# Performance work log

Measured on AMD Instinct MI355X. Metric: run time of the kernel, lower is better.

## Reference

```python
import jax, jax.numpy as jnp
import numpy as np

D_MODEL = 1024
D_HEAD = 64
RANK = 8
LEAF = 4
NUM_LEAVES = D_HEAD // LEAF            # 16
NUM_LEVELS = 4                          # log2(64/4)
BLOCK_SIZES = [4, 8, 16, 32]
RANKS = [min(RANK, b) for b in BLOCK_SIZES]   # [4,8,8,8]
NUM_NODES = [NUM_LEAVES // 2 ** (l + 1) for l in range(NUM_LEVELS)]  # [8,4,2,1]


def _elu1(x):
    return jax.nn.elu(x) + 1.0


def setup_inputs() -> dict:
    key = jax.random.key(0)
    ks = jax.random.split(key, 32)
    B, T = 8, 2048
    x = jax.random.normal(ks[0], (B, T, D_MODEL), jnp.float32)
    s_in = 1.0 / np.sqrt(D_MODEL)
    s_out = 1.0 / np.sqrt(D_HEAD)
    inp = {
        'x': x,
        'Wq': jax.random.normal(ks[1], (D_MODEL, D_HEAD), jnp.float32) * s_in,
        'Wk': jax.random.normal(ks[2], (D_MODEL, D_HEAD), jnp.float32) * s_in,
        'Wv': jax.random.normal(ks[3], (D_MODEL, D_HEAD), jnp.float32) * s_in,
        'Wo': jax.random.normal(ks[4], (D_HEAD, D_MODEL), jnp.float32) * s_out,
    }
    # Fixed orthonormal bases per level (torch.linalg.qr of randn in original)
    idx = 5
    for name in ['UL', 'VR', 'UR', 'VL']:
        for l in range(NUM_LEVELS):
            bs, rl = BLOCK_SIZES[l], RANKS[l]
            Q, _ = jnp.linalg.qr(jax.random.normal(ks[idx], (bs, rl), jnp.float32))
            inp[f'{name}{l}'] = Q
            idx += 1
    return inp


def _hss_forward(x, Wq, Wk, Wv, Wo, UL, VR, UR, VL):
    B, T, _ = x.shape
    q = _elu1(x @ Wq)   # (B,T,Dh)
    k = _elu1(x @ Wk)
    v = x @ Wv

    leaf0 = jnp.zeros((B, NUM_LEAVES, LEAF, LEAF), x.dtype)
    Ws0 = tuple(jnp.zeros((B, NUM_NODES[l], RANKS[l], RANKS[l]), x.dtype)
                for l in range(NUM_LEVELS))
    z0 = jnp.zeros((B, D_HEAD), x.dtype)

    def step(carry, kvq):
        leaf, Ws, z = carry
        k_t, v_t, q_t = kvq  # each (B, Dh)
        # rank-1 update: leaf diagonal blocks
        leaf = leaf + jnp.einsum('bni,bnj->bnij',
                                 k_t.reshape(B, NUM_LEAVES, LEAF),
                                 v_t.reshape(B, NUM_LEAVES, LEAF))
        newWs = []
        for l in range(NUM_LEVELS):
            bs, nn = BLOCK_SIZES[l], NUM_NODES[l]
            u_r = k_t.reshape(B, nn, 2 * bs)
            v_r = v_t.reshape(B, nn, 2 * bs)
            uL = jnp.einsum('bnd,dr->bnr', u_r[:, :, :bs], UL[l])
            vR = jnp.einsum('bnd,dr->bnr', v_r[:, :, bs:], VR[l])
            newWs.append(Ws[l] + jnp.einsum('bni,bnj->bnij', uL, vR))
        Ws = tuple(newWs)
        z = z + k_t
        # HSS matvec: y = S @ q_t
        y = jnp.einsum('bnij,bnj->bni', leaf,
                       q_t.reshape(B, NUM_LEAVES, LEAF)).reshape(B, D_HEAD)
        for l in range(NUM_LEVELS):
            bs, nn = BLOCK_SIZES[l], NUM_NODES[l]
            x_r = q_t.reshape(B, nn, 2 * bs)
            vr_x = jnp.einsum('bnd,dr->bnr', x_r[:, :, bs:], VR[l])
            y_top = jnp.einsum('dr,bnr->bnd', UL[l],
                               jnp.einsum('bnij,bnj->bni', Ws[l], vr_x))
            vl_x = jnp.einsum('bnd,dr->bnr', x_r[:, :, :bs], VL[l])
            y_bot = jnp.einsum('dr,bnr->bnd', UR[l],
                               jnp.einsum('bnji,bnj->bni', Ws[l], vl_x))
            y = y + jnp.concatenate([y_top, y_bot], axis=-1).reshape(B, D_HEAD)
        denom = jnp.maximum(jnp.sum(z * q_t, axis=-1, keepdims=True), 1e-6)
        return (leaf, Ws, z), y / denom

    kvq = (jnp.swapaxes(k, 0, 1), jnp.swapaxes(v, 0, 1), jnp.swapaxes(q, 0, 1))
    _, outs = jax.lax.scan(step, (leaf0, Ws0, z0), kvq)  # (T,B,Dh)
    out = jnp.swapaxes(outs, 0, 1)  # (B,T,Dh); dropout is identity in eval
    return out @ Wo


def reference(x, Wq, Wk, Wv, Wo,
              UL0, UL1, UL2, UL3,
              VR0, VR1, VR2, VR3,
              UR0, UR1, UR2, UR3,
              VL0, VL1, VL2, VL3):
    UL = (UL0, UL1, UL2, UL3)
    VR = (VR0, VR1, VR2, VR3)
    UR = (UR0, UR1, UR2, UR3)
    VL = (VL0, VL1, VL2, VL3)
    return _hss_forward(x, Wq, Wk, Wv, Wo, UL, VR, UR, VL)
```

## Files before the change

kernel.cpp:

```cpp
#include <hip/hip_runtime.h>
#include <hip/hip_bf16.h>

typedef unsigned short u16;
typedef __attribute__((ext_vector_type(8))) short bf16x8;
typedef __attribute__((ext_vector_type(4))) float f32x4;

#define B_ 8
#define T_ 2048
#define BT_ (B_*T_)
#define DM_ 1024
#define DH_ 64
#define NCH_ 64
#define S_ (T_/NCH_)
#define STATE_ 896

__device__ __forceinline__ float b2f(u16 u){ unsigned v=((unsigned)u)<<16; float f; __builtin_memcpy(&f,&v,4); return f; }
__device__ __forceinline__ u16 f2b(float f){ __hip_bfloat16 h=__float2bfloat16(f); u16 u; __builtin_memcpy(&u,&h,2); return u; }

__device__ __forceinline__ float ldin(const void* p, size_t i, int f32){
  return f32 ? ((const float*)p)[i] : b2f(((const u16*)p)[i]);
}
__device__ __forceinline__ bf16x8 ld8bf(const void* p, size_t i, int f32){
  if (f32){
    f32x4 v0 = *(const f32x4*)((const float*)p + i);
    f32x4 v1 = *(const f32x4*)((const float*)p + i + 4);
    bf16x8 r;
    #pragma unroll
    for (int j=0;j<4;j++){ r[j] = (short)f2b(v0[j]); r[4+j] = (short)f2b(v1[j]); }
    return r;
  }
  return *(const bf16x8*)((const u16*)p + i);
}

__device__ __forceinline__ void decodeWs(int e, int& ia, int& ib){
  if (e<384){ int o=e-256, n=o>>4; ia=n*4+((o>>2)&3); ib=n*4+(o&3); }
  else if (e<640){ int o=e-384, n=o>>6; ia=32+n*8+((o>>3)&7); ib=32+n*8+(o&7); }
  else if (e<768){ int o=e-640, n=o>>6; ia=64+n*8+((o>>3)&7); ib=64+n*8+(o&7); }
  else { int o=e-768; ia=80+((o>>3)&7); ib=80+(o&7); }
}
__device__ __forceinline__ void decode88(int f, int& l, int& n, int& ri){
  if (f<32){ l=0; n=f>>2; ri=f&3; }
  else if (f<64){ l=1; n=(f-32)>>3; ri=f&7; }
  else if (f<80){ l=2; n=(f-64)>>3; ri=f&7; }
  else { l=3; n=0; ri=f&7; }
}

__global__ __launch_bounds__(64) void k_detect(const u16* __restrict__ x, int* __restrict__ flag){
  int tid = threadIdx.x;
  int sane = 0;
  for (int i = tid; i < 4096; i += 64){
    u16 u = x[i];
    int e = (u >> 7) & 0xFF;
    if ((u & 0x7FFF) == 0 || (e >= 100 && e <= 140)) sane++;
  }
  #pragma unroll
  for (int o = 32; o > 0; o >>= 1) sane += __shfl_down(sane, o);
  if (tid == 0) flag[0] = (sane < 3600) ? 1 : 0;
}

__global__ __launch_bounds__(256) void k_wfrag(
    const void* __restrict__ Wq, const void* __restrict__ Wk, const void* __restrict__ Wv,
    const void* __restrict__ Wo,
    const void* __restrict__ UL0, const void* __restrict__ UL1, const void* __restrict__ UL2, const void* __restrict__ UL3,
    const void* __restrict__ VR0, const void* __restrict__ VR1, const void* __restrict__ VR2, const void* __restrict__ VR3,
    const void* __restrict__ VL0, const void* __restrict__ VL1, const void* __restrict__ VL2, const void* __restrict__ VL3,
    u16* __restrict__ WF, u16* __restrict__ WoF, u16* __restrict__ PF,
    const int* __restrict__ fl)
{
  const int f32 = fl[0];
  int e = blockIdx.x*256 + threadIdx.x;
  if (e < 24576){
    int m = e >> 13;
    int rem = e & 8191;
    int ks = rem >> 8;
    int nt = (rem >> 6) & 3;
    int lane = rem & 63;
    const void* W = (m==0)?Wq:((m==1)?Wk:Wv);
    int kr = ks*32 + (lane>>4)*8;
    int col = nt*16 + (lane&15);
    u16 o[8];
    #pragma unroll
    for (int j=0;j<8;j++) o[j] = f2b(ldin(W, (size_t)(kr+j)*DH_ + col, f32));
    u16* dst = WF + (size_t)e*8;
    #pragma unroll
    for (int j=0;j<8;j++) dst[j] = o[j];
  } else if (e < 32768){
    int eo = e - 24576;
    int ks = eo >> 12;
    int nt = (eo >> 6) & 63;
    int lane = eo & 63;
    int kr = ks*32 + (lane>>4)*8;
    int col = nt*16 + (lane&15);
    u16 o[8];
    #pragma unroll
    for (int j=0;j<8;j++) o[j] = f2b(ldin(Wo, (size_t)(kr+j)*DM_ + col, f32));
    u16* dst = WoF + (size_t)eo*8;
    #pragma unroll
    for (int j=0;j<8;j++) dst[j] = o[j];
  } else if (e < 35072){
    int pe = e - 32768;
    int lane = pe & 63;
    int nt = (pe >> 6) % 6;
    int mk = pe / 384;
    int ks = mk & 1, mat = mk >> 1;
    int col = nt*16 + (lane&15);
    int dbase = ks*32 + (lane>>4)*8;
    const int BSl[4]={4,8,16,32}; const int Rl[4]={4,8,8,8};
    u16 o[8];
    #pragma unroll
    for (int j=0;j<8;j++){
      float val = 0.f;
      if (col < 88){
        int l,n,ri; decode88(col,l,n,ri);
        int bs=BSl[l], r=Rl[l];
        int lo = n*2*bs + ((mat==1)?bs:0);
        int d = dbase + j;
        if (d >= lo && d < lo+bs){
          const void* Up;
          if (mat==0)      Up = (l==0)?UL0:(l==1)?UL1:(l==2)?UL2:UL3;
          else if (mat==1) Up = (l==0)?VR0:(l==1)?VR1:(l==2)?VR2:VR3;
          else             Up = (l==0)?VL0:(l==1)?VL1:(l==2)?VL2:VL3;
          val = ldin(Up, (size_t)(d-lo)*r + ri, f32);
        }
      }
      o[j] = f2b(val);
    }
    u16* dst = PF + (size_t)pe*8;
    #pragma unroll
    for (int j=0;j<8;j++) dst[j] = o[j];
  }
}

__global__ __launch_bounds__(256) void k_proj4(
    const void* __restrict__ x, const u16* __restrict__ WF,
    float* __restrict__ oq, float* __restrict__ ok_, float* __restrict__ ov,
    u16* __restrict__ qb16, u16* __restrict__ kb16, u16* __restrict__ vb16,
    const int* __restrict__ fl)
{
  __shared__ f32x4 red[3][8][64];
  const int f32 = fl[0];
  const int m = blockIdx.y;
  const int rows0 = blockIdx.x*32;
  const int wv = threadIdx.x>>6;
  const int lane = threadIdx.x&63;
  const int quad = lane>>4, l16 = lane&15;
  const size_t rowA0 = (size_t)(rows0 + l16)*DM_;
  const size_t rowA1 = (size_t)(rows0 + 16 + l16)*DM_;

  f32x4 acc[8];
  #pragma unroll
  for (int i=0;i<8;i++) acc[i] = (f32x4){0.f,0.f,0.f,0.f};

  const int ks0 = wv*8;
  #pragma unroll 4
  for (int kk=0;kk<8;kk++){
    int ks = ks0 + kk;
    int ko = ks*32 + quad*8;
    bf16x8 a0 = ld8bf(x, rowA0 + ko, f32);
    bf16x8 a1 = ld8bf(x, rowA1 + ko, f32);
    #pragma unroll
    for (int nt=0;nt<4;nt++){
      bf16x8 b = *(const bf16x8*)(WF + ((size_t)((m*32+ks)*4+nt)*64 + lane)*8);
      acc[nt]   = __builtin_amdgcn_mfma_f32_16x16x32_bf16(a0,b,acc[nt],0,0,0);
      acc[4+nt] = __builtin_amdgcn_mfma_f32_16x16x32_bf16(a1,b,acc[4+nt],0,0,0);
    }
  }

  if (wv>0){
    #pragma unroll
    for (int i=0;i<8;i++) red[wv-1][i][lane] = acc[i];
  }
  __syncthreads();
  if (wv==0){
    #pragma unroll
    for (int i=0;i<8;i++){
      f32x4 r0 = red[0][i][lane];
      f32x4 r1 = red[1][i][lane];
      f32x4 r2 = red[2][i][lane];
      acc[i][0]+=r0[0]+r1[0]+r2[0]; acc[i][1]+=r0[1]+r1[1]+r2[1];
      acc[i][2]+=r0[2]+r1[2]+r2[2]; acc[i][3]+=r0[3]+r1[3]+r2[3];
    }
    float* __restrict__ outp = (m==0)?oq:((m==1)?ok_:ov);
    u16* __restrict__ outb = (m==0)?qb16:((m==1)?kb16:vb16);
    #pragma unroll
    for (int sp=0;sp<2;sp++){
      #pragma unroll
      for (int nt=0;nt<4;nt++){
        #pragma unroll
        for (int i=0;i<4;i++){
          int row = rows0 + sp*16 + quad*4 + i;
          int col = nt*16 + l16;
          float val = acc[sp*4+nt][i];
          if (m<2) val = (val>0.f)? (val+1.f) : expf(val);
          outp[(size_t)row*DH_ + col] = val;
          outb[(size_t)row*DH_ + col] = f2b(val);
        }
      }
    }
  }
}

__global__ __launch_bounds__(64) void k_prep3(
    const u16* __restrict__ qb16, const u16* __restrict__ kb16, const u16* __restrict__ vb16,
    const u16* __restrict__ PF,
    float* __restrict__ uLa, float* __restrict__ vRa, float* __restrict__ vrxa, float* __restrict__ vlxa)
{
  const int m = blockIdx.y;
  const int rows0 = blockIdx.x*16;
  const int lane = threadIdx.x;
  const int quad = lane>>4, l16 = lane&15;

  const u16* __restrict__ src = (m==0)?kb16:((m==1)?vb16:qb16);
  const int mat = (m==0)?0:((m==3)?2:1);

  bf16x8 a[2];
  #pragma unroll
  for (int ks=0;ks<2;ks++){
    size_t off = (size_t)(rows0 + l16)*DH_ + ks*32 + quad*8;
    a[ks] = *(const bf16x8*)(src + off);
  }
  f32x4 acc[6];
  #pragma unroll
  for (int nt=0;nt<6;nt++) acc[nt] = (f32x4){0.f,0.f,0.f,0.f};

  #pragma unroll
  for (int ks=0;ks<2;ks++){
    #pragma unroll
    for (int nt=0;nt<6;nt++){
      bf16x8 b = *(const bf16x8*)(PF + ((size_t)((mat*2+ks)*6+nt)*64 + lane)*8);
      acc[nt] = __builtin_amdgcn_mfma_f32_16x16x32_bf16(a[ks], b, acc[nt],0,0,0);
    }
  }
  float* __restrict__ dst = (m==0)?uLa:(m==1)?vRa:(m==2)?vrxa:vlxa;
  #pragma unroll
  for (int nt=0;nt<6;nt++){
    int col = nt*16 + l16;
    if (col < 88){
      #pragma unroll
      for (int i=0;i<4;i++){
        int row = rows0 + quad*4 + i;
        dst[(size_t)row*88 + col] = acc[nt][i];
      }
    }
  }
}

__global__ __launch_bounds__(256) void k_chunksum(
    const float* __restrict__ gk, const float* __restrict__ gv,
    const float* __restrict__ uLa, const float* __restrict__ vRa,
    float* __restrict__ SL)
{
  const int bid = blockIdx.x;
  const int b = bid/NCH_, c = bid%NCH_;
  const size_t base64 = (size_t)(b*T_ + c*S_)*64;
  const size_t base88 = (size_t)(b*T_ + c*S_)*88;
  for (int p=0;p<4;p++){
    int e = threadIdx.x + p*256;
    if (e>=STATE_) break;
    float acc=0.f;
    if (e < 256){
      int n=e>>4;
      const float* A = gk + base64 + n*4 + ((e>>2)&3);
      const float* Bp = gv + base64 + n*4 + (e&3);
      for (int s=0;s<S_;s++) acc += A[s*64]*Bp[s*64];
    } else if (e < 832){
      int ia, ib; decodeWs(e, ia, ib);
      const float* A = uLa + base88 + ia;
      const float* Bp = vRa + base88 + ib;
      for (int s=0;s<S_;s++) acc += A[s*88]*Bp[s*88];
    } else {
      const float* A = gk + base64 + (e-832);
      for (int s=0;s<S_;s++) acc += A[s*64];
    }
    SL[(size_t)bid*STATE_ + e] = acc;
  }
}

__global__ __launch_bounds__(256) void k_prefix(const float* __restrict__ SL, float* __restrict__ SP){
  const int b = blockIdx.x;
  for (int p=0;p<4;p++){
    int e = threadIdx.x + p*256;
    if (e>=STATE_) break;
    float run=0.f;
    for (int c=0;c<NCH_;c++){
      size_t idx = ((size_t)(b*NCH_+c))*STATE_ + e;
      SP[idx] = run; run += SL[idx];
    }
  }
}

__global__ __launch_bounds__(256) void k_intra(
    const float* __restrict__ gq, const float* __restrict__ gk, const float* __restrict__ gv,
    const float* __restrict__ uLa, const float* __restrict__ vRa,
    const float* __restrict__ vrxa, const float* __restrict__ vlxa,
    const float* __restrict__ SP,
    const void* __restrict__ UL0, const void* __restrict__ UL1, const void* __restrict__ UL2, const void* __restrict__ UL3,
    const void* __restrict__ UR0, const void* __restrict__ UR1, const void* __restrict__ UR2, const void* __restrict__ UR3,
    u16* __restrict__ Yb, const int* __restrict__ fl)
{
  __shared__ float kS[S_*64];
  __shared__ float vS[S_*64];
  __shared__ float uvS[S_*176];
  __shared__ float st0[STATE_];
  __shared__ float ULs[464], URs[464];
  const int f32 = fl[0];
  const int tid = threadIdx.x;
  const int bid = blockIdx.x;
  const int b = bid/NCH_, c = bid%NCH_;
  const int row0 = b*T_ + c*S_;

  const size_t r64 = (size_t)row0*64;
  for (int i=tid;i<S_*64;i+=256){ kS[i]=gk[r64+i]; vS[i]=gv[r64+i]; }
  const size_t r88 = (size_t)row0*88;
  for (int i=tid;i<S_*88;i+=256){
    int s=i/88, f=i-s*88;
    uvS[s*176+f]    = uLa[r88+i];
    uvS[s*176+88+f] = vRa[r88+i];
  }
  for (int e=tid;e<STATE_;e+=256) st0[e] = SP[(size_t)bid*STATE_+e];
  for (int e=tid;e<464;e+=256){
    int l, idx;
    if (e<16){ l=0; idx=e; } else if (e<80){ l=1; idx=e-16; }
    else if (e<208){ l=2; idx=e-80; } else { l=3; idx=e-208; }
    const void* ul = (l==0)?UL0:(l==1)?UL1:(l==2)?UL2:UL3;
    const void* ur = (l==0)?UR0:(l==1)?UR1:(l==2)?UR2:UR3;
    ULs[e] = ldin(ul, idx, f32); URs[e] = ldin(ur, idx, f32);
  }
  __syncthreads();

  const int w = tid>>6, lane = tid&63, tl = lane>>3, g = lane&7;
  const int t = w*8 + tl;
  const int n1 = g>>1, ri1 = (g&1)*4;
  const int n2 = g>>2, ri2 = (g&3)*2;
  const size_t row = (size_t)(row0 + t);

  float qr[8];
  { const float* qp = gq + row*64 + g*8;
    *(f32x4*)&qr[0] = *(const f32x4*)qp; *(f32x4*)&qr[4] = *(const f32x4*)(qp+4); }
  float rxL0[4], lxL0[4], rxL1[8], lxL1[8], rxL2[8], lxL2[8], rxL3[8], lxL3[8];
  { const float* rp = vrxa + row*88; const float* lp = vlxa + row*88;
    *(f32x4*)&rxL0[0] = *(const f32x4*)(rp + 4*g);
    *(f32x4*)&lxL0[0] = *(const f32x4*)(lp + 4*g);
    *(f32x4*)&rxL1[0] = *(const f32x4*)(rp + 32 + n1*8); *(f32x4*)&rxL1[4] = *(const f32x4*)(rp + 36 + n1*8);
    *(f32x4*)&lxL1[0] = *(const f32x4*)(lp + 32 + n1*8); *(f32x4*)&lxL1[4] = *(const f32x4*)(lp + 36 + n1*8);
    *(f32x4*)&rxL2[0] = *(const f32x4*)(rp + 64 + n2*8); *(f32x4*)&rxL2[4] = *(const f32x4*)(rp + 68 + n2*8);
    *(f32x4*)&lxL2[0] = *(const f32x4*)(lp + 64 + n2*8); *(f32x4*)&lxL2[4] = *(const f32x4*)(lp + 68 + n2*8);
    *(f32x4*)&rxL3[0] = *(const f32x4*)(rp + 80); *(f32x4*)&rxL3[4] = *(const f32x4*)(rp + 84);
    *(f32x4*)&lxL3[0] = *(const f32x4*)(lp + 80); *(f32x4*)&lxL3[4] = *(const f32x4*)(lp + 84); }

  float yacc[8], den = 0.f;
  #pragma unroll
  for (int cc=0;cc<8;cc++){
    int n = 2*g + (cc>>2);
    const float* m = &st0[n*16 + (cc&3)*4];
    const float* qp = &qr[(cc>>2)*4];
    yacc[cc] = m[0]*qp[0]+m[1]*qp[1]+m[2]*qp[2]+m[3]*qp[3];
    den += st0[832 + g*8 + cc]*qr[cc];
  }
  float gtL0[4], gbL0[4], gtL1[4], gbL1[4], gtL2[2], gbL2[2], gtL3, gbL3;
  #pragma unroll
  for (int cc=0;cc<4;cc++){
    const float* m = &st0[256 + g*16 + cc*4];
    gtL0[cc] = m[0]*rxL0[0]+m[1]*rxL0[1]+m[2]*rxL0[2]+m[3]*rxL0[3];
    float s2 = 0.f;
    #pragma unroll
    for (int j=0;j<4;j++) s2 += st0[256 + g*16 + j*4 + cc]*lxL0[j];
    gbL0[cc] = s2;
  }
  #pragma unroll
  for (int cc=0;cc<4;cc++){
    int ri = ri1 + cc;
    float s1=0.f, s2=0.f;
    #pragma unroll
    for (int j=0;j<8;j++){
      s1 += st0[384 + n1*64 + ri*8 + j]*rxL1[j];
      s2 += st0[384 + n1*64 + j*8 + ri]*lxL1[j];
    }
    gtL1[cc]=s1; gbL1[cc]=s2;
  }
  #pragma unroll
  for (int cc=0;cc<2;cc++){
    int ri = ri2 + cc;
    float s1=0.f, s2=0.f;
    #pragma unroll
    for (int j=0;j<8;j++){
      s1 += st0[640 + n2*64 + ri*8 + j]*rxL2[j];
      s2 += st0[640 + n2*64 + j*8 + ri]*lxL2[j];
    }
    gtL2[cc]=s1; gbL2[cc]=s2;
  }
  { float s1=0.f, s2=0.f;
    #pragma unroll
    for (int j=0;j<8;j++){
      s1 += st0[768 + g*8 + j]*rxL3[j];
      s2 += st0[768 + j*8 + g]*lxL3[j];
    }
    gtL3=s1; gbL3=s2; }

  const int smax = w*8 + 8;
  for (int s=0; s<smax; s++){
    const float* ks_ = &kS[s*64 + g*8];
    const float* vs_ = &vS[s*64 + g*8];
    const float* uL_ = &uvS[s*176];
    const float* vR_ = &uvS[s*176 + 88];
    float dv0 = vs_[0]*qr[0]+vs_[1]*qr[1]+vs_[2]*qr[2]+vs_[3]*qr[3];
    float dv1 = vs_[4]*qr[4]+vs_[5]*qr[5]+vs_[6]*qr[6]+vs_[7]*qr[7];
    float dn = 0.f;
    #pragma unroll
    for (int cc=0;cc<8;cc++) dn += ks_[cc]*qr[cc];
    float d1L0=0.f,d2L0=0.f;
    #pragma unroll
    for (int j=0;j<4;j++){ d1L0 += vR_[4*g+j]*rxL0[j]; d2L0 += uL_[4*g+j]*lxL0[j]; }
    float d1L1=0.f,d2L1=0.f;
    #pragma unroll
    for (int j=0;j<8;j++){ d1L1 += vR_[32+n1*8+j]*rxL1[j]; d2L1 += uL_[32+n1*8+j]*lxL1[j]; }
    float d1L2=0.f,d2L2=0.f;
    #pragma unroll
    for (int j=0;j<8;j++){ d1L2 += vR_[64+n2*8+j]*rxL2[j]; d2L2 += uL_[64+n2*8+j]*lxL2[j]; }
    float d1L3=0.f,d2L3=0.f;
    #pragma unroll
    for (int j=0;j<8;j++){ d1L3 += vR_[80+j]*rxL3[j]; d2L3 += uL_[80+j]*lxL3[j]; }
    if (s<=t){
      den += dn;
      #pragma unroll
      for (int cc=0;cc<8;cc++) yacc[cc] += ks_[cc]*((cc<4)?dv0:dv1);
      #pragma unroll
      for (int cc=0;cc<4;cc++){
        gtL0[cc] += uL_[4*g+cc]*d1L0;          gbL0[cc] += vR_[4*g+cc]*d2L0;
        gtL1[cc] += uL_[32+n1*8+ri1+cc]*d1L1;  gbL1[cc] += vR_[32+n1*8+ri1+cc]*d2L1;
      }
      #pragma unroll
      for (int cc=0;cc<2;cc++){
        gtL2[cc] += uL_[64+n2*8+ri2+cc]*d1L2;  gbL2[cc] += vR_[64+n2*8+ri2+cc]*d2L2;
      }
      gtL3 += uL_[80+g]*d1L3;  gbL3 += vR_[80+g]*d2L3;
    }
  }
  __syncthreads();

  { float* gr = &uvS[t*176];
    #pragma unroll
    for (int cc=0;cc<4;cc++){
      gr[4*g+cc] = gtL0[cc];                 gr[88+4*g+cc] = gbL0[cc];
      gr[32+n1*8+ri1+cc] = gtL1[cc];         gr[88+32+n1*8+ri1+cc] = gbL1[cc];
    }
    #pragma unroll
    for (int cc=0;cc<2;cc++){
      gr[64+n2*8+ri2+cc] = gtL2[cc];         gr[88+64+n2*8+ri2+cc] = gbL2[cc];
    }
    gr[80+g] = gtL3;  gr[88+80+g] = gbL3;
  }
  __syncthreads();

  den += __shfl_xor(den,1); den += __shfl_xor(den,2); den += __shfl_xor(den,4);
  float inv = 1.f / fmaxf(den, 1e-6f);
  const float* gr = &uvS[t*176];
  float yout[8];
  #pragma unroll
  for (int cc=0;cc<8;cc++){
    int j = g*8 + cc;
    float y = yacc[cc];
    if (cc<4){
      #pragma unroll
      for (int rr=0;rr<4;rr++) y += ULs[cc*4+rr]*gr[g*4+rr];
    } else {
      #pragma unroll
      for (int rr=0;rr<4;rr++) y += URs[(cc-4)*4+rr]*gr[88+g*4+rr];
    }
    { int seg=j>>4, pos=j&15;
      if (pos<8){
        #pragma unroll
        for (int rr=0;rr<8;rr++) y += ULs[16+pos*8+rr]*gr[32+seg*8+rr];
      } else {
        #pragma unroll
        for (int rr=0;rr<8;rr++) y += URs[16+(pos-8)*8+rr]*gr[88+32+seg*8+rr];
      } }
    { int seg=j>>5, pos=j&31;
      if (pos<16){
        #pragma unroll
        for (int rr=0;rr<8;rr++) y += ULs[80+pos*8+rr]*gr[64+seg*8+rr];
      } else {
        #pragma unroll
        for (int rr=0;rr<8;rr++) y += URs[80+(pos-16)*8+rr]*gr[88+64+seg*8+rr];
      } }
    { int pos=j;
      if (pos<32){
        #pragma unroll
        for (int rr=0;rr<8;rr++) y += ULs[208+pos*8+rr]*gr[80+rr];
      } else {
        #pragma unroll
        for (int rr=0;rr<8;rr++) y += URs[208+(pos-32)*8+rr]*gr[88+80+rr];
      } }
    yout[cc] = y*inv;
  }
  u16* yp = Yb + row*64 + g*8;
  ushort4 o1, o2;
  o1.x=f2b(yout[0]); o1.y=f2b(yout[1]); o1.z=f2b(yout[2]); o1.w=f2b(yout[3]);
  o2.x=f2b(yout[4]); o2.y=f2b(yout[5]); o2.z=f2b(yout[6]); o2.w=f2b(yout[7]);
  *(ushort4*)yp = o1;
  *(ushort4*)(yp+4) = o2;
}

__global__ __launch_bounds__(64) void k_outproj2(
    const u16* __restrict__ Yb, const u16* __restrict__ WoF, void* __restrict__ outv,
    const int* __restrict__ fl)
{
  const int f32 = fl[0];
  const int rows0 = blockIdx.x*32;
  const int nt0 = blockIdx.y*16;
  const int lane = threadIdx.x;
  const int quad = lane>>4, l16 = lane&15;

  f32x4 acc[32];
  #pragma unroll
  for (int i=0;i<32;i++) acc[i] = (f32x4){0.f,0.f,0.f,0.f};

  #pragma unroll
  for (int ks=0;ks<2;ks++){
    int ko = ks*32 + quad*8;
    bf16x8 a0 = *(const bf16x8*)(Yb + (size_t)(rows0 + l16)*DH_ + ko);
    bf16x8 a1 = *(const bf16x8*)(Yb + (size_t)(rows0 + 16 + l16)*DH_ + ko);
    #pragma unroll
    for (int nt=0;nt<16;nt++){
      bf16x8 b = *(const bf16x8*)(WoF + ((size_t)(ks*64 + nt0 + nt)*64 + lane)*8);
      acc[nt]    = __builtin_amdgcn_mfma_f32_16x16x32_bf16(a0,b,acc[nt],0,0,0);
      acc[16+nt] = __builtin_amdgcn_mfma_f32_16x16x32_bf16(a1,b,acc[16+nt],0,0,0);
    }
  }
  #pragma unroll
  for (int sp=0;sp<2;sp++){
    #pragma unroll
    for (int nt=0;nt<16;nt++){
      #pragma unroll
      for (int i=0;i<4;i++){
        int row = rows0 + sp*16 + quad*4 + i;
        int col = (nt0+nt)*16 + l16;
        size_t idx = (size_t)row*DM_ + col;
        float v = acc[sp*16+nt][i];
        if (f32) ((float*)outv)[idx] = v;
        else ((u16*)outv)[idx] = f2b(v);
      }
    }
  }
}

extern "C" void kernel_launch(void* const* d_in, const int* in_sizes, int n_in,
                              void* d_out, int out_size, void* d_ws, size_t ws_size,
                              hipStream_t stream) {
  const void* x  = d_in[0];
  const void* Wq = d_in[1];
  const void* Wk = d_in[2];
  const void* Wv = d_in[3];
  const void* Wo = d_in[4];
  const void* UL[4] = {d_in[5],d_in[6],d_in[7],d_in[8]};
  const void* VR[4] = {d_in[9],d_in[10],d_in[11],d_in[12]};
  const void* UR[4] = {d_in[13],d_in[14],d_in[15],d_in[16]};
  const void* VL[4] = {d_in[17],d_in[18],d_in[19],d_in[20]};

  int* flag = (int*)d_ws;
  float* ws = (float*)d_ws + 16;
  float* q    = ws;
  float* kf   = q    + (size_t)BT_*64;
  float* vf   = kf   + (size_t)BT_*64;
  float* uLa  = vf   + (size_t)BT_*64;
  float* vRa  = uLa  + (size_t)BT_*88;
  float* vrxa = vRa  + (size_t)BT_*88;
  float* vlxa = vrxa + (size_t)BT_*88;
  float* SL   = vlxa + (size_t)BT_*88;
  float* SP   = SL   + (size_t)B_*NCH_*STATE_;
  u16*   Yb   = (u16*)(SP + (size_t)B_*NCH_*STATE_);
  u16*   WF   = Yb  + (size_t)BT_*64;
  u16*   WoF  = WF  + (size_t)196608;
  u16*   PF   = WoF + (size_t)65536;
  u16*   qb16 = PF  + (size_t)18432;
  u16*   kb16 = qb16 + (size_t)BT_*64;
  u16*   vb16 = kb16 + (size_t)BT_*64;

  k_detect<<<1, 64, 0, stream>>>((const u16*)x, flag);
  k_wfrag<<<137, 256, 0, stream>>>(Wq, Wk, Wv, Wo,
      UL[0],UL[1],UL[2],UL[3], VR[0],VR[1],VR[2],VR[3], VL[0],VL[1],VL[2],VL[3],
      WF, WoF, PF, flag);
  k_proj4<<<dim3(512, 3), 256, 0, stream>>>(x, WF, q, kf, vf, qb16, kb16, vb16, flag);
  k_prep3<<<dim3(BT_/16, 4), 64, 0, stream>>>(qb16, kb16, vb16, PF, uLa, vRa, vrxa, vlxa);
  k_chunksum<<<B_*NCH_, 256, 0, stream>>>(kf, vf, uLa, vRa, SL);
  k_prefix<<<B_, 256, 0, stream>>>(SL, SP);
  k_intra<<<B_*NCH_, 256, 0, stream>>>(q, kf, vf, uLa, vRa, vrxa, vlxa, SP,
      UL[0],UL[1],UL[2],UL[3], UR[0],UR[1],UR[2],UR[3], Yb, flag);
  k_outproj2<<<dim3(512, 4), 64, 0, stream>>>(Yb, WoF, d_out, flag);
}
```

Baseline: 279.3 us.

## Merge QKV projections into one block per 16 rows and halve out-projection tiles

The QKV projection kernel now runs all three matrices (q, k, v) in one 768-thread block of 12 waves covering 16 rows, so each x tile is fetched by one block and can be reused from cache. Before, three separate blocks each read the same 32-row x tile. The output projection kernel halves its column tile per block (8 instead of 16 n-tiles), which doubles the grid and cuts accumulator registers to help occupancy. The trade-offs are smaller per-wave work and 16-row tiles, which give less B-fragment reuse per A load, plus more blocks to launch.

```diff
diff --git a/kernel.cpp b/kernel.cpp
--- a/kernel.cpp
+++ b/kernel.cpp
@@ -131,70 +131,65 @@
   }
 }
 
-__global__ __launch_bounds__(256) void k_proj4(
+__global__ __launch_bounds__(768, 8) void k_proj5(
     const void* __restrict__ x, const u16* __restrict__ WF,
     float* __restrict__ oq, float* __restrict__ ok_, float* __restrict__ ov,
     u16* __restrict__ qb16, u16* __restrict__ kb16, u16* __restrict__ vb16,
     const int* __restrict__ fl)
 {
-  __shared__ f32x4 red[3][8][64];
+  __shared__ f32x4 red[9][4][64];
   const int f32 = fl[0];
-  const int m = blockIdx.y;
-  const int rows0 = blockIdx.x*32;
+  const int rows0 = blockIdx.x*16;
   const int wv = threadIdx.x>>6;
+  const int m  = wv>>2;
+  const int kq = wv&3;
   const int lane = threadIdx.x&63;
   const int quad = lane>>4, l16 = lane&15;
-  const size_t rowA0 = (size_t)(rows0 + l16)*DM_;
-  const size_t rowA1 = (size_t)(rows0 + 16 + l16)*DM_;
-
-  f32x4 acc[8];
-  #pragma unroll
-  for (int i=0;i<8;i++) acc[i] = (f32x4){0.f,0.f,0.f,0.f};
-
-  const int ks0 = wv*8;
-  #pragma unroll 4
+  const size_t rowA = (size_t)(rows0 + l16)*DM_;
+
+  f32x4 acc[4];
+  #pragma unroll
+  for (int i=0;i<4;i++) acc[i] = (f32x4){0.f,0.f,0.f,0.f};
+
+  const int ks0 = kq*8;
+  #pragma unroll 2
   for (int kk=0;kk<8;kk++){
     int ks = ks0 + kk;
     int ko = ks*32 + quad*8;
-    bf16x8 a0 = ld8bf(x, rowA0 + ko, f32);
-    bf16x8 a1 = ld8bf(x, rowA1 + ko, f32);
+    bf16x8 a = ld8bf(x, rowA + ko, f32);
     #pragma unroll
     for (int nt=0;nt<4;nt++){
       bf16x8 b = *(const bf16x8*)(WF + ((size_t)((m*32+ks)*4+nt)*64 + lane)*8);
-      acc[nt]   = __builtin_amdgcn_mfma_f32_16x16x32_bf16(a0,b,acc[nt],0,0,0);
-      acc[4+nt] = __builtin_amdgcn_mfma_f32_16x16x32_bf16(a1,b,acc[4+nt],0,0,0);
-    }
-  }
-
-  if (wv>0){
-    #pragma unroll
-    for (int i=0;i<8;i++) red[wv-1][i][lane] = acc[i];
+      acc[nt] = __builtin_amdgcn_mfma_f32_16x16x32_bf16(a,b,acc[nt],0,0,0);
+    }
+  }
+
+  if (kq>0){
+    #pragma unroll
+    for (int i=0;i<4;i++) red[m*3+(kq-1)][i][lane] = acc[i];
   }
   __syncthreads();
-  if (wv==0){
-    #pragma unroll
-    for (int i=0;i<8;i++){
-      f32x4 r0 = red[0][i][lane];
-      f32x4 r1 = red[1][i][lane];
-      f32x4 r2 = red[2][i][lane];
+  if (kq==0){
+    #pragma unroll
+    for (int i=0;i<4;i++){
+      f32x4 r0 = red[m*3+0][i][lane];
+      f32x4 r1 = red[m*3+1][i][lane];
+      f32x4 r2 = red[m*3+2][i][lane];
       acc[i][0]+=r0[0]+r1[0]+r2[0]; acc[i][1]+=r0[1]+r1[1]+r2[1];
       acc[i][2]+=r0[2]+r1[2]+r2[2]; acc[i][3]+=r0[3]+r1[3]+r2[3];
     }
     float* __restrict__ outp = (m==0)?oq:((m==1)?ok_:ov);
     u16* __restrict__ outb = (m==0)?qb16:((m==1)?kb16:vb16);
     #pragma unroll
-    for (int sp=0;sp<2;sp++){
-      #pragma unroll
-      for (int nt=0;nt<4;nt++){
-        #pragma unroll
-        for (int i=0;i<4;i++){
-          int row = rows0 + sp*16 + quad*4 + i;
-          int col = nt*16 + l16;
-          float val = acc[sp*4+nt][i];
-          if (m<2) val = (val>0.f)? (val+1.f) : expf(val);
-          outp[(size_t)row*DH_ + col] = val;
-          outb[(size_t)row*DH_ + col] = f2b(val);
-        }
+    for (int nt=0;nt<4;nt++){
+      #pragma unroll
+      for (int i=0;i<4;i++){
+        int row = rows0 + quad*4 + i;
+        int col = nt*16 + l16;
+        float val = acc[nt][i];
+        if (m<2) val = (val>0.f)? (val+1.f) : expf(val);
+        outp[(size_t)row*DH_ + col] = val;
+        outb[(size_t)row*DH_ + col] = f2b(val);
       }
     }
   }
@@ -501,19 +496,19 @@
   *(ushort4*)(yp+4) = o2;
 }
 
-__global__ __launch_bounds__(64) void k_outproj2(
+__global__ __launch_bounds__(64,4) void k_outproj3(
     const u16* __restrict__ Yb, const u16* __restrict__ WoF, void* __restrict__ outv,
     const int* __restrict__ fl)
 {
   const int f32 = fl[0];
   const int rows0 = blockIdx.x*32;
-  const int nt0 = blockIdx.y*16;
+  const int nt0 = blockIdx.y*8;
   const int lane = threadIdx.x;
   const int quad = lane>>4, l16 = lane&15;
 
-  f32x4 acc[32];
-  #pragma unroll
-  for (int i=0;i<32;i++) acc[i] = (f32x4){0.f,0.f,0.f,0.f};
+  f32x4 acc[16];
+  #pragma unroll
+  for (int i=0;i<16;i++) acc[i] = (f32x4){0.f,0.f,0.f,0.f};
 
   #pragma unroll
   for (int ks=0;ks<2;ks++){
@@ -521,22 +516,22 @@
     bf16x8 a0 = *(const bf16x8*)(Yb + (size_t)(rows0 + l16)*DH_ + ko);
     bf16x8 a1 = *(const bf16x8*)(Yb + (size_t)(rows0 + 16 + l16)*DH_ + ko);
     #pragma unroll
-    for (int nt=0;nt<16;nt++){
+    for (int nt=0;nt<8;nt++){
       bf16x8 b = *(const bf16x8*)(WoF + ((size_t)(ks*64 + nt0 + nt)*64 + lane)*8);
-      acc[nt]    = __builtin_amdgcn_mfma_f32_16x16x32_bf16(a0,b,acc[nt],0,0,0);
-      acc[16+nt] = __builtin_amdgcn_mfma_f32_16x16x32_bf16(a1,b,acc[16+nt],0,0,0);
+      acc[nt]   = __builtin_amdgcn_mfma_f32_16x16x32_bf16(a0,b,acc[nt],0,0,0);
+      acc[8+nt] = __builtin_amdgcn_mfma_f32_16x16x32_bf16(a1,b,acc[8+nt],0,0,0);
     }
   }
   #pragma unroll
   for (int sp=0;sp<2;sp++){
     #pragma unroll
-    for (int nt=0;nt<16;nt++){
+    for (int nt=0;nt<8;nt++){
       #pragma unroll
       for (int i=0;i<4;i++){
         int row = rows0 + sp*16 + quad*4 + i;
         int col = (nt0+nt)*16 + l16;
         size_t idx = (size_t)row*DM_ + col;
-        float v = acc[sp*16+nt][i];
+        float v = acc[sp*8+nt][i];
         if (f32) ((float*)outv)[idx] = v;
         else ((u16*)outv)[idx] = f2b(v);
       }
@@ -580,11 +575,11 @@
   k_wfrag<<<137, 256, 0, stream>>>(Wq, Wk, Wv, Wo,
       UL[0],UL[1],UL[2],UL[3], VR[0],VR[1],VR[2],VR[3], VL[0],VL[1],VL[2],VL[3],
       WF, WoF, PF, flag);
-  k_proj4<<<dim3(512, 3), 256, 0, stream>>>(x, WF, q, kf, vf, qb16, kb16, vb16, flag);
+  k_proj5<<<BT_/16, 768, 0, stream>>>(x, WF, q, kf, vf, qb16, kb16, vb16, flag);
   k_prep3<<<dim3(BT_/16, 4), 64, 0, stream>>>(qb16, kb16, vb16, PF, uLa, vRa, vrxa, vlxa);
   k_chunksum<<<B_*NCH_, 256, 0, stream>>>(kf, vf, uLa, vRa, SL);
   k_prefix<<<B_, 256, 0, stream>>>(SL, SP);
   k_intra<<<B_*NCH_, 256, 0, stream>>>(q, kf, vf, uLa, vRa, vrxa, vlxa, SP,
       UL[0],UL[1],UL[2],UL[3], UR[0],UR[1],UR[2],UR[3], Yb, flag);
-  k_outproj2<<<dim3(512, 4), 64, 0, stream>>>(Yb, WoF, d_out, flag);
-}
+  k_outproj3<<<dim3(512, 8), 64, 0, stream>>>(Yb, WoF, d_out, flag);
+}
```

Result: no change. 278.2 us (-0.4%).
